# Kernel optimization log

Measured on AMD Instinct MI355X. Metric: run time of the kernel, lower is better.

The kernel has to match this reference:

```python
import jax, jax.numpy as jnp
import numpy as np

B, T, F, U = 32768, 7, 36, 256

def setup_inputs() -> dict:
    key = jax.random.key(0)
    ks = jax.random.split(key, 5)
    x = jax.random.normal(ks[0], (B, T, F), dtype=jnp.float32)
    h0 = jax.random.normal(ks[1], (B, U), dtype=jnp.float32)
    c0 = jax.random.normal(ks[2], (B, U), dtype=jnp.float32)
    Wk = jax.random.normal(ks[3], (F, 4 * U), dtype=jnp.float32) * 0.1
    Wr = jax.random.normal(ks[4], (U, 4 * U), dtype=jnp.float32) * 0.05
    b = jnp.zeros((4 * U,), dtype=jnp.float32)
    return {"x": x, "h0": h0, "c0": c0, "Wk": Wk, "Wr": Wr, "b": b}

def reference(x, h0, c0, Wk, Wr, b):
    # Precompute input projection for all 7 steps: [B,T,4U]
    zx = jnp.einsum('btf,fg->btg', x, Wk) + b
    zx_t = jnp.transpose(zx, (1, 0, 2))  # time-major [T,B,4U]

    def step(carry, z_in):
        h, c = carry
        z = z_in + h @ Wr  # [B,4U]
        i, f, g, o = jnp.split(z, 4, axis=-1)  # Keras gate order i,f,g,o
        i = jax.nn.sigmoid(i)
        f = jax.nn.sigmoid(f)
        g = jnp.tanh(g)
        o = jax.nn.sigmoid(o)
        c_new = f * c + i * g
        h_new = o * jnp.tanh(c_new)
        return (h_new, c_new), h_new

    (_, _), hs = jax.lax.scan(step, (h0, c0), zx_t)
    return jnp.transpose(hs, (1, 0, 2))  # [B,T,U] (return_sequences=True)
```

## Files before the change

kernel.cpp:

```cpp
#include <hip/hip_runtime.h>
#include <hip/hip_bf16.h>

typedef _Float16 half8 __attribute__((ext_vector_type(8)));
typedef float f32x4 __attribute__((ext_vector_type(4)));

#define B_TOTAL 32768
#define T 7
#define F 36
#define U 256
#define G4 1024
#define BM 64
#define KC 10
#define KPACK 32
#define H_STRIDE 264
#define X_STRIDE 72

__global__ __launch_bounds__(1024) void pack_w(const float* __restrict__ Wr,
                                               const float* __restrict__ Wk,
                                               _Float16* __restrict__ Wq) {
    const int kc   = blockIdx.x >> 2;
    const int kin0 = (blockIdx.x & 3) * 8;
    const int n    = threadIdx.x;
    _Float16* dst = Wq + ((size_t)kc * G4 + n) * KPACK + kin0;
    #pragma unroll
    for (int j = 0; j < 8; ++j) {
        int k = kc * KPACK + kin0 + j;
        float v = 0.f;
        if (k < U)          v = Wr[(size_t)k * G4 + n];
        else if (k < U + F) v = Wk[(size_t)(k - U) * G4 + n];
        dst[j] = (_Float16)v;
    }
}

__device__ __forceinline__ float fast_sigmoid(float x) {
    return __builtin_amdgcn_rcpf(1.f + __expf(-x));
}
__device__ __forceinline__ float fast_tanh(float x) {
    return 1.f - 2.f * __builtin_amdgcn_rcpf(1.f + __expf(2.f * x));
}

__global__ __launch_bounds__(1024) void lstm_kernel(
    const float* __restrict__ x,
    const float* __restrict__ h0,
    const float* __restrict__ c0,
    const _Float16* __restrict__ Wq,
    const float* __restrict__ bias_g,
    float* __restrict__ out)
{
    __shared__ __align__(16) _Float16 hA[BM * H_STRIDE];
    __shared__ __align__(16) _Float16 xA[BM * X_STRIDE];

    const int tid  = threadIdx.x;
    const int lane = tid & 63;
    const int w    = tid >> 6;
    const int l15  = lane & 15;
    const int q    = lane >> 4;
    const int u0   = w * 16;
    const int b0   = blockIdx.x * BM;

    for (int i = tid; i < BM * U; i += 1024) {
        int m = i >> 8, u = i & 255;
        hA[m * H_STRIDE + u] = (_Float16)h0[(size_t)b0 * U + i];
    }
    for (int i = tid; i < BM * (64 - F); i += 1024) {
        int m = i / (64 - F), f = i % (64 - F);
        xA[m * X_STRIDE + F + f] = (_Float16)0.f;
    }
    for (int i = tid; i < BM * F; i += 1024) {
        int m = i / F, f = i % F;
        xA[m * X_STRIDE + f] = (_Float16)x[((size_t)(b0 + m) * T) * F + f];
    }
    float c[16];
    #pragma unroll
    for (int mt = 0; mt < 4; ++mt)
        #pragma unroll
        for (int r = 0; r < 4; ++r) {
            int row = mt * 16 + q * 4 + r;
            c[mt * 4 + r] = c0[(size_t)(b0 + row) * U + u0 + l15];
        }
    float bv[4];
    #pragma unroll
    for (int g = 0; g < 4; ++g) bv[g] = bias_g[g * U + u0 + l15];

    __syncthreads();

    for (int t = 0; t < T; ++t) {
        f32x4 acc[4][4];
        #pragma unroll
        for (int mt = 0; mt < 4; ++mt)
            #pragma unroll
            for (int g = 0; g < 4; ++g)
                acc[mt][g] = (f32x4){bv[g], bv[g], bv[g], bv[g]};

        float xp0 = 0.f, xp1 = 0.f, xp2 = 0.f;
        if (t + 1 < T) {
            {
                int i = tid;        int m = i / F, f = i % F;
                xp0 = x[((size_t)(b0 + m) * T + t + 1) * F + f];
            }
            {
                int i = tid + 1024; int m = i / F, f = i % F;
                xp1 = x[((size_t)(b0 + m) * T + t + 1) * F + f];
            }
            if (tid < BM * F - 2048) {
                int i = tid + 2048; int m = i / F, f = i % F;
                xp2 = x[((size_t)(b0 + m) * T + t + 1) * F + f];
            }
        }

        #pragma unroll 2
        for (int kc = 0; kc < KC; ++kc) {
            half8 bf[4];
            #pragma unroll
            for (int g = 0; g < 4; ++g) {
                size_t off = ((size_t)kc * G4 + g * U + u0 + l15) * KPACK + q * 8;
                bf[g] = *(const half8*)(Wq + off);
            }
            #pragma unroll
            for (int mt = 0; mt < 4; ++mt) {
                half8 af;
                if (kc < 8)
                    af = *(const half8*)&hA[(mt * 16 + l15) * H_STRIDE + kc * 32 + q * 8];
                else
                    af = *(const half8*)&xA[(mt * 16 + l15) * X_STRIDE + (kc - 8) * 32 + q * 8];
                #pragma unroll
                for (int g = 0; g < 4; ++g)
                    acc[mt][g] = __builtin_amdgcn_mfma_f32_16x16x32_f16(af, bf[g], acc[mt][g], 0, 0, 0);
            }
        }

        float hnew[16];
        #pragma unroll
        for (int mt = 0; mt < 4; ++mt)
            #pragma unroll
            for (int r = 0; r < 4; ++r) {
                float zi = acc[mt][0][r];
                float zf = acc[mt][1][r];
                float zg = acc[mt][2][r];
                float zo = acc[mt][3][r];
                float ig = fast_sigmoid(zi);
                float fg = fast_sigmoid(zf);
                float gg = fast_tanh(zg);
                float og = fast_sigmoid(zo);
                float cn = fg * c[mt * 4 + r] + ig * gg;
                c[mt * 4 + r] = cn;
                hnew[mt * 4 + r] = og * fast_tanh(cn);
            }

        __syncthreads();

        #pragma unroll
        for (int mt = 0; mt < 4; ++mt)
            #pragma unroll
            for (int r = 0; r < 4; ++r) {
                int row = mt * 16 + q * 4 + r;
                hA[row * H_STRIDE + u0 + l15] = (_Float16)hnew[mt * 4 + r];
            }
        if (t + 1 < T) {
            { int i = tid;        int m = i / F, f = i % F; xA[m * X_STRIDE + f] = (_Float16)xp0; }
            { int i = tid + 1024; int m = i / F, f = i % F; xA[m * X_STRIDE + f] = (_Float16)xp1; }
            if (tid < BM * F - 2048) {
                int i = tid + 2048; int m = i / F, f = i % F;
                xA[m * X_STRIDE + f] = (_Float16)xp2;
            }
        }
        __syncthreads();

        #pragma unroll
        for (int rb = 0; rb < 2; ++rb) {
            int j   = tid + rb * 1024;
            int row = j >> 5;
            int uo  = (j & 31) * 8;
            half8 hv = *(const half8*)&hA[row * H_STRIDE + uo];
            f32x4 lo = { (float)hv[0], (float)hv[1], (float)hv[2], (float)hv[3] };
            f32x4 hi = { (float)hv[4], (float)hv[5], (float)hv[6], (float)hv[7] };
            float* dst = out + ((size_t)(b0 + row) * T + t) * U + uo;
            *(f32x4*)dst       = lo;
            *(f32x4*)(dst + 4) = hi;
        }
    }
}

extern "C" void kernel_launch(void* const* d_in, const int* in_sizes, int n_in,
                              void* d_out, int out_size, void* d_ws, size_t ws_size,
                              hipStream_t stream) {
    const float* x  = (const float*)d_in[0];
    const float* h0 = (const float*)d_in[1];
    const float* c0 = (const float*)d_in[2];
    const float* Wk = (const float*)d_in[3];
    const float* Wr = (const float*)d_in[4];
    const float* b  = (const float*)d_in[5];
    float* out = (float*)d_out;

    _Float16* Wq = (_Float16*)d_ws;

    pack_w<<<KC * 4, 1024, 0, stream>>>(Wr, Wk, Wq);
    lstm_kernel<<<B_TOTAL / BM, 1024, 0, stream>>>(x, h0, c0, Wq, b, out);
}
```

Baseline: 517.2 us.

## Halve batch tile, double-buffer LDS state, fold bias into packed weights

Cuts the batch tile from 64 to 32 rows and the block from 1024 to 512 threads. Each wave now covers 32 hidden units and 2 row tiles, so every global weight fragment feeds two MFMAs instead of four, and more blocks can sit on each CU. The h and x shared buffers are double-buffered, which removes one __syncthreads per step and lets h be written straight to LDS from the gate epilogue. The bias becomes an extra K row of the packed weights, fed by a constant 1 in the padded x columns, so the per-thread bias loads and initialisation go away. In exchange, weight traffic per row doubles and the bias is rounded to fp16.

```diff
diff --git a/kernel.cpp b/kernel.cpp
--- a/kernel.cpp
+++ b/kernel.cpp
@@ -9,14 +9,17 @@
 #define F 36
 #define U 256
 #define G4 1024
-#define BM 64
+#define BM 32
+#define NTHREADS 512
 #define KC 10
 #define KPACK 32
+#define K_BIAS 316
 #define H_STRIDE 264
 #define X_STRIDE 72
 
 __global__ __launch_bounds__(1024) void pack_w(const float* __restrict__ Wr,
                                                const float* __restrict__ Wk,
+                                               const float* __restrict__ bias,
                                                _Float16* __restrict__ Wq) {
     const int kc   = blockIdx.x >> 2;
     const int kin0 = (blockIdx.x & 3) * 8;
@@ -26,8 +29,9 @@
     for (int j = 0; j < 8; ++j) {
         int k = kc * KPACK + kin0 + j;
         float v = 0.f;
-        if (k < U)          v = Wr[(size_t)k * G4 + n];
-        else if (k < U + F) v = Wk[(size_t)(k - U) * G4 + n];
+        if (k < U)            v = Wr[(size_t)k * G4 + n];
+        else if (k < U + F)   v = Wk[(size_t)(k - U) * G4 + n];
+        else if (k == K_BIAS) v = bias[n];
         dst[j] = (_Float16)v;
     }
 }
@@ -39,139 +43,134 @@
     return 1.f - 2.f * __builtin_amdgcn_rcpf(1.f + __expf(2.f * x));
 }
 
-__global__ __launch_bounds__(1024) void lstm_kernel(
+__global__ __launch_bounds__(NTHREADS, 4) void lstm_kernel(
     const float* __restrict__ x,
     const float* __restrict__ h0,
     const float* __restrict__ c0,
     const _Float16* __restrict__ Wq,
-    const float* __restrict__ bias_g,
     float* __restrict__ out)
 {
-    __shared__ __align__(16) _Float16 hA[BM * H_STRIDE];
-    __shared__ __align__(16) _Float16 xA[BM * X_STRIDE];
+    __shared__ __align__(16) _Float16 hA[2][BM * H_STRIDE];
+    __shared__ __align__(16) _Float16 xA[2][BM * X_STRIDE];
 
     const int tid  = threadIdx.x;
     const int lane = tid & 63;
     const int w    = tid >> 6;
     const int l15  = lane & 15;
     const int q    = lane >> 4;
-    const int u0   = w * 16;
+    const int u0   = w * 32;
     const int b0   = blockIdx.x * BM;
 
-    for (int i = tid; i < BM * U; i += 1024) {
+    for (int i = tid; i < BM * U; i += NTHREADS) {
         int m = i >> 8, u = i & 255;
-        hA[m * H_STRIDE + u] = (_Float16)h0[(size_t)b0 * U + i];
+        hA[0][m * H_STRIDE + u] = (_Float16)h0[(size_t)b0 * U + i];
     }
-    for (int i = tid; i < BM * (64 - F); i += 1024) {
-        int m = i / (64 - F), f = i % (64 - F);
-        xA[m * X_STRIDE + F + f] = (_Float16)0.f;
+    for (int i = tid; i < 2 * BM * (64 - F); i += NTHREADS) {
+        int buf = i / (BM * (64 - F));
+        int j   = i % (BM * (64 - F));
+        int m = j / (64 - F), f = F + j % (64 - F);
+        xA[buf][m * X_STRIDE + f] = (f == (K_BIAS - U)) ? (_Float16)1.f : (_Float16)0.f;
     }
-    for (int i = tid; i < BM * F; i += 1024) {
+    for (int i = tid; i < BM * F; i += NTHREADS) {
         int m = i / F, f = i % F;
-        xA[m * X_STRIDE + f] = (_Float16)x[((size_t)(b0 + m) * T) * F + f];
+        xA[0][m * X_STRIDE + f] = (_Float16)x[((size_t)(b0 + m) * T) * F + f];
     }
     float c[16];
     #pragma unroll
-    for (int mt = 0; mt < 4; ++mt)
+    for (int mt = 0; mt < 2; ++mt)
         #pragma unroll
-        for (int r = 0; r < 4; ++r) {
-            int row = mt * 16 + q * 4 + r;
-            c[mt * 4 + r] = c0[(size_t)(b0 + row) * U + u0 + l15];
-        }
-    float bv[4];
-    #pragma unroll
-    for (int g = 0; g < 4; ++g) bv[g] = bias_g[g * U + u0 + l15];
+        for (int us = 0; us < 2; ++us)
+            #pragma unroll
+            for (int r = 0; r < 4; ++r) {
+                int row = mt * 16 + q * 4 + r;
+                c[(mt * 2 + us) * 4 + r] = c0[(size_t)(b0 + row) * U + u0 + us * 16 + l15];
+            }
 
     __syncthreads();
 
     for (int t = 0; t < T; ++t) {
-        f32x4 acc[4][4];
+        const int p = t & 1;
+        f32x4 acc[2][2][4];
         #pragma unroll
-        for (int mt = 0; mt < 4; ++mt)
+        for (int mt = 0; mt < 2; ++mt)
             #pragma unroll
-            for (int g = 0; g < 4; ++g)
-                acc[mt][g] = (f32x4){bv[g], bv[g], bv[g], bv[g]};
+            for (int us = 0; us < 2; ++us)
+                #pragma unroll
+                for (int g = 0; g < 4; ++g)
+                    acc[mt][us][g] = (f32x4){0.f, 0.f, 0.f, 0.f};
 
         float xp0 = 0.f, xp1 = 0.f, xp2 = 0.f;
         if (t + 1 < T) {
-            {
-                int i = tid;        int m = i / F, f = i % F;
-                xp0 = x[((size_t)(b0 + m) * T + t + 1) * F + f];
-            }
-            {
+            { int i = tid;       int m = i / F, f = i % F;
+              xp0 = x[((size_t)(b0 + m) * T + t + 1) * F + f]; }
+            { int i = tid + 512; int m = i / F, f = i % F;
+              xp1 = x[((size_t)(b0 + m) * T + t + 1) * F + f]; }
+            if (tid < BM * F - 1024) {
                 int i = tid + 1024; int m = i / F, f = i % F;
-                xp1 = x[((size_t)(b0 + m) * T + t + 1) * F + f];
-            }
-            if (tid < BM * F - 2048) {
-                int i = tid + 2048; int m = i / F, f = i % F;
                 xp2 = x[((size_t)(b0 + m) * T + t + 1) * F + f];
             }
         }
 
-        #pragma unroll 2
+        #pragma unroll
         for (int kc = 0; kc < KC; ++kc) {
-            half8 bf[4];
+            half8 af[2];
+            if (kc < 8) {
+                af[0] = *(const half8*)&hA[p][(l15)      * H_STRIDE + kc * 32 + q * 8];
+                af[1] = *(const half8*)&hA[p][(16 + l15) * H_STRIDE + kc * 32 + q * 8];
+            } else {
+                af[0] = *(const half8*)&xA[p][(l15)      * X_STRIDE + (kc - 8) * 32 + q * 8];
+                af[1] = *(const half8*)&xA[p][(16 + l15) * X_STRIDE + (kc - 8) * 32 + q * 8];
+            }
             #pragma unroll
             for (int g = 0; g < 4; ++g) {
-                size_t off = ((size_t)kc * G4 + g * U + u0 + l15) * KPACK + q * 8;
-                bf[g] = *(const half8*)(Wq + off);
-            }
-            #pragma unroll
-            for (int mt = 0; mt < 4; ++mt) {
-                half8 af;
-                if (kc < 8)
-                    af = *(const half8*)&hA[(mt * 16 + l15) * H_STRIDE + kc * 32 + q * 8];
-                else
-                    af = *(const half8*)&xA[(mt * 16 + l15) * X_STRIDE + (kc - 8) * 32 + q * 8];
-                #pragma unroll
-                for (int g = 0; g < 4; ++g)
-                    acc[mt][g] = __builtin_amdgcn_mfma_f32_16x16x32_f16(af, bf[g], acc[mt][g], 0, 0, 0);
+                half8 bf0 = *(const half8*)(Wq + ((size_t)kc * G4 + g * U + u0 + l15)      * KPACK + q * 8);
+                half8 bf1 = *(const half8*)(Wq + ((size_t)kc * G4 + g * U + u0 + 16 + l15) * KPACK + q * 8);
+                acc[0][0][g] = __builtin_amdgcn_mfma_f32_16x16x32_f16(af[0], bf0, acc[0][0][g], 0, 0, 0);
+                acc[0][1][g] = __builtin_amdgcn_mfma_f32_16x16x32_f16(af[0], bf1, acc[0][1][g], 0, 0, 0);
+                acc[1][0][g] = __builtin_amdgcn_mfma_f32_16x16x32_f16(af[1], bf0, acc[1][0][g], 0, 0, 0);
+                acc[1][1][g] = __builtin_amdgcn_mfma_f32_16x16x32_f16(af[1], bf1, acc[1][1][g], 0, 0, 0);
             }
         }
 
-        float hnew[16];
         #pragma unroll
-        for (int mt = 0; mt < 4; ++mt)
+        for (int mt = 0; mt < 2; ++mt)
             #pragma unroll
-            for (int r = 0; r < 4; ++r) {
-                float zi = acc[mt][0][r];
-                float zf = acc[mt][1][r];
-                float zg = acc[mt][2][r];
-                float zo = acc[mt][3][r];
-                float ig = fast_sigmoid(zi);
-                float fg = fast_sigmoid(zf);
-                float gg = fast_tanh(zg);
-                float og = fast_sigmoid(zo);
-                float cn = fg * c[mt * 4 + r] + ig * gg;
-                c[mt * 4 + r] = cn;
-                hnew[mt * 4 + r] = og * fast_tanh(cn);
+            for (int us = 0; us < 2; ++us)
+                #pragma unroll
+                for (int r = 0; r < 4; ++r) {
+                    int ci = (mt * 2 + us) * 4 + r;
+                    float zi = acc[mt][us][0][r];
+                    float zf = acc[mt][us][1][r];
+                    float zg = acc[mt][us][2][r];
+                    float zo = acc[mt][us][3][r];
+                    float ig = fast_sigmoid(zi);
+                    float fg = fast_sigmoid(zf);
+                    float gg = fast_tanh(zg);
+                    float og = fast_sigmoid(zo);
+                    float cn = fg * c[ci] + ig * gg;
+                    c[ci] = cn;
+                    float hv = og * fast_tanh(cn);
+                    int row = mt * 16 + q * 4 + r;
+                    hA[p ^ 1][row * H_STRIDE + u0 + us * 16 + l15] = (_Float16)hv;
+                }
+
+        if (t + 1 < T) {
+            { int i = tid;       int m = i / F, f = i % F; xA[p ^ 1][m * X_STRIDE + f] = (_Float16)xp0; }
+            { int i = tid + 512; int m = i / F, f = i % F; xA[p ^ 1][m * X_STRIDE + f] = (_Float16)xp1; }
+            if (tid < BM * F - 1024) {
+                int i = tid + 1024; int m = i / F, f = i % F;
+                xA[p ^ 1][m * X_STRIDE + f] = (_Float16)xp2;
             }
+        }
 
         __syncthreads();
 
         #pragma unroll
-        for (int mt = 0; mt < 4; ++mt)
-            #pragma unroll
-            for (int r = 0; r < 4; ++r) {
-                int row = mt * 16 + q * 4 + r;
-                hA[row * H_STRIDE + u0 + l15] = (_Float16)hnew[mt * 4 + r];
-            }
-        if (t + 1 < T) {
-            { int i = tid;        int m = i / F, f = i % F; xA[m * X_STRIDE + f] = (_Float16)xp0; }
-            { int i = tid + 1024; int m = i / F, f = i % F; xA[m * X_STRIDE + f] = (_Float16)xp1; }
-            if (tid < BM * F - 2048) {
-                int i = tid + 2048; int m = i / F, f = i % F;
-                xA[m * X_STRIDE + f] = (_Float16)xp2;
-            }
-        }
-        __syncthreads();
-
-        #pragma unroll
         for (int rb = 0; rb < 2; ++rb) {
-            int j   = tid + rb * 1024;
+            int j   = tid + rb * NTHREADS;
             int row = j >> 5;
             int uo  = (j & 31) * 8;
-            half8 hv = *(const half8*)&hA[row * H_STRIDE + uo];
+            half8 hv = *(const half8*)&hA[p ^ 1][row * H_STRIDE + uo];
             f32x4 lo = { (float)hv[0], (float)hv[1], (float)hv[2], (float)hv[3] };
             f32x4 hi = { (float)hv[4], (float)hv[5], (float)hv[6], (float)hv[7] };
             float* dst = out + ((size_t)(b0 + row) * T + t) * U + uo;
@@ -194,6 +193,6 @@
 
     _Float16* Wq = (_Float16*)d_ws;
 
-    pack_w<<<KC * 4, 1024, 0, stream>>>(Wr, Wk, Wq);
-    lstm_kernel<<<B_TOTAL / BM, 1024, 0, stream>>>(x, h0, c0, Wq, b, out);
+    pack_w<<<KC * 4, 1024, 0, stream>>>(Wr, Wk, b, Wq);
+    lstm_kernel<<<B_TOTAL / BM, NTHREADS, 0, stream>>>(x, h0, c0, Wq, out);
 }
```

Result: slower. 1.388 ms (+168.4%).
